# Performance work log

Measured on AMD Instinct MI355X. Metric: run time of the kernel, lower is better.

## Reference

```python
import jax, jax.numpy as jnp
import numpy as np

N, D = 8192, 128
ALPHA = 2.0


def setup_inputs() -> dict:
    key = jax.random.key(0)
    k1, k2, k3, k4 = jax.random.split(key, 4)
    z_au = jax.random.normal(k1, (N, D), dtype=jnp.float32)
    z_tp = jax.random.normal(k2, (N, D), dtype=jnp.float32)
    fc_weights = jax.random.normal(k3, (2, D), dtype=jnp.float32)
    labels = jax.random.randint(k4, (N,), 0, 2, dtype=jnp.int64)
    return {"z_au": z_au, "z_tp": z_tp, "fc_weights": fc_weights, "labels": labels}


def reference(z_au, z_tp, fc_weights, labels):
    # labels is unused in the (intended) math; kept for signature fidelity.
    n = z_au.shape[0]
    neg_inf = jnp.finfo(z_au.dtype).min
    eye = jnp.eye(n, dtype=bool)

    # pairwise dot-product similarities (cosim == raw matmul in the source)
    s_aa = z_au @ z_au.T              # [n, n]
    s_tt = z_tp @ z_tp.T              # [n, n]
    s_at = z_au @ z_tp.T              # [n, n]

    # pos_loss(i) = log( sum_{j!=i} exp(au_i.au_j) + exp(tp_i.tp_j) )
    pos_logits = jnp.concatenate(
        [jnp.where(eye, neg_inf, s_aa), jnp.where(eye, neg_inf, s_tt)], axis=1
    )                                  # [n, 2n]
    pos = jax.nn.logsumexp(pos_logits, axis=1)          # [n]

    # neg_loss(i) = log( sum_{j!=i} exp(au_i.tp_j) )
    neg = jax.nn.logsumexp(jnp.where(eye, neg_inf, s_at), axis=1)  # [n]

    # alpha * cosim(au_i, tp_i)
    au_tp_diag = jnp.einsum("nd,nd->n", z_au, z_tp)      # [n]

    supcon = jnp.sum(-pos + neg + ALPHA * au_tp_diag)

    # prototype loss: reward same-class prototype, punish other-class prototype
    pt0, pt1 = fc_weights[0], fc_weights[1]
    pt_loss = jnp.sum(-z_au @ pt0 + z_au @ pt1 - z_tp @ pt1 + z_tp @ pt0) / n

    return (pt_loss + supcon) / (n + 2)
```

## Files before the change

### kernel.cpp

```cpp
#include <hip/hip_runtime.h>


typedef float f32x4 __attribute__((ext_vector_type(4)));
typedef __bf16 bf16x8 __attribute__((ext_vector_type(8)));

static constexpr int   N_ROWS = 8192;
static constexpr int   DIM    = 128;
static constexpr float SQRT_LOG2E = 1.2011224087864498f;
static constexpr float C2  = 32.0f;
static constexpr float LN2 = 0.6931471805599453f;


__device__ inline unsigned short f2bf_rne(float x) {
    unsigned u = __builtin_bit_cast(unsigned, x);
    u += 0x7fffu + ((u >> 16) & 1u);
    return (unsigned short)(u >> 16);
}

__global__ void prep_kernel(const float* __restrict__ zau,
                            const float* __restrict__ ztp,
                            unsigned short* __restrict__ bau,
                            unsigned short* __restrict__ btp,
                            float* __restrict__ P, float* __restrict__ Ng,
                            float* __restrict__ acc) {
    int gid  = blockIdx.x * blockDim.x + threadIdx.x;
    int base = gid * 4;
    float4 a = *reinterpret_cast<const float4*>(zau + base);
    float4 t = *reinterpret_cast<const float4*>(ztp + base);
    ushort4 ua, ut;
    ua.x = f2bf_rne(a.x * SQRT_LOG2E); ua.y = f2bf_rne(a.y * SQRT_LOG2E);
    ua.z = f2bf_rne(a.z * SQRT_LOG2E); ua.w = f2bf_rne(a.w * SQRT_LOG2E);
    ut.x = f2bf_rne(t.x * SQRT_LOG2E); ut.y = f2bf_rne(t.y * SQRT_LOG2E);
    ut.z = f2bf_rne(t.z * SQRT_LOG2E); ut.w = f2bf_rne(t.w * SQRT_LOG2E);
    *reinterpret_cast<ushort4*>(bau + base) = ua;
    *reinterpret_cast<ushort4*>(btp + base) = ut;
    if (gid < N_ROWS) { P[gid] = 0.0f; Ng[gid] = 0.0f; }
    if (gid == 0)     { acc[0] = 0.0f; acc[1] = 0.0f; }
}

template<bool DIAG>
__device__ inline void accum_exp(const f32x4 (&acc)[2][4], float (&dst)[2][4],
                                 int r0w, int colbase, int quad, int l15) {
#pragma unroll
    for (int mt = 0; mt < 2; mt++)
#pragma unroll
        for (int nt = 0; nt < 4; nt++)
#pragma unroll
            for (int r = 0; r < 4; r++) {
                float e = __builtin_amdgcn_exp2f(acc[mt][nt][r]);
                if (DIAG) {
                    int grow = r0w + mt * 16 + quad * 4 + r;
                    int gcol = colbase + nt * 16 + l15;
                    if (grow == gcol) e = 0.0f;
                }
                dst[mt][r] += e;
            }
}

__global__ __launch_bounds__(256, 2)
void score_kernel(const unsigned short* __restrict__ bau,
                  const unsigned short* __restrict__ btp,
                  float* __restrict__ P, float* __restrict__ Ng) {
    __shared__ __align__(16) unsigned short ldsA[64 * 136];
    __shared__ __align__(16) unsigned short ldsT[64 * 136];

    const int tid  = threadIdx.x;
    const int lane = tid & 63;
    const int wave = tid >> 6;
    const int quad = lane >> 4;
    const int l15  = lane & 15;
    const int rb   = blockIdx.x >> 3;
    const int cs   = blockIdx.x & 7;
    const int r0w  = rb * 128 + wave * 32;

    bf16x8 aAu[2][4], aTp[2][4];
#pragma unroll
    for (int mt = 0; mt < 2; mt++) {
        int row = r0w + mt * 16 + l15;
        const unsigned short* pa = bau + row * DIM + quad * 8;
        const unsigned short* pt = btp + row * DIM + quad * 8;
#pragma unroll
        for (int k = 0; k < 4; k++) {
            aAu[mt][k] = *reinterpret_cast<const bf16x8*>(pa + k * 32);
            aTp[mt][k] = *reinterpret_cast<const bf16x8*>(pt + k * 32);
        }
    }

    float sP[2][4] = {{0.f,0.f,0.f,0.f},{0.f,0.f,0.f,0.f}};
    float sN[2][4] = {{0.f,0.f,0.f,0.f},{0.f,0.f,0.f,0.f}};

    for (int ct = 0; ct < 16; ct++) {
        const int colbase = cs * 1024 + ct * 64;
        __syncthreads();
#pragma unroll
        for (int j = 0; j < 8; j++) {
            int c   = tid + j * 256;
            int arr = c >> 10;
            int rem = c & 1023;
            int row = rem >> 4;
            int c16 = rem & 15;
            const unsigned short* src =
                (arr ? btp : bau) + (colbase + row) * DIM + c16 * 8;
            unsigned short* dst = (arr ? ldsT : ldsA) + row * 136 + c16 * 8;
            *reinterpret_cast<bf16x8*>(dst) =
                *reinterpret_cast<const bf16x8*>(src);
        }
        __syncthreads();

        const bool diag = (colbase < r0w + 32) && (colbase + 64 > r0w);

        {
            f32x4 acc[2][4];
#pragma unroll
            for (int mt = 0; mt < 2; mt++)
#pragma unroll
                for (int nt = 0; nt < 4; nt++)
                    acc[mt][nt] = f32x4{-C2, -C2, -C2, -C2};
#pragma unroll
            for (int k = 0; k < 4; k++) {
                bf16x8 b[4];
#pragma unroll
                for (int nt = 0; nt < 4; nt++)
                    b[nt] = *reinterpret_cast<const bf16x8*>(
                        ldsA + (nt * 16 + l15) * 136 + k * 32 + quad * 8);
#pragma unroll
                for (int nt = 0; nt < 4; nt++)
#pragma unroll
                    for (int mt = 0; mt < 2; mt++)
                        acc[mt][nt] = __builtin_amdgcn_mfma_f32_16x16x32_bf16(
                            aAu[mt][k], b[nt], acc[mt][nt], 0, 0, 0);
            }
            if (diag) accum_exp<true >(acc, sP, r0w, colbase, quad, l15);
            else      accum_exp<false>(acc, sP, r0w, colbase, quad, l15);
        }

        {
            f32x4 accT[2][4], accX[2][4];
#pragma unroll
            for (int mt = 0; mt < 2; mt++)
#pragma unroll
                for (int nt = 0; nt < 4; nt++) {
                    accT[mt][nt] = f32x4{-C2, -C2, -C2, -C2};
                    accX[mt][nt] = f32x4{-C2, -C2, -C2, -C2};
                }
#pragma unroll
            for (int k = 0; k < 4; k++) {
                bf16x8 b[4];
#pragma unroll
                for (int nt = 0; nt < 4; nt++)
                    b[nt] = *reinterpret_cast<const bf16x8*>(
                        ldsT + (nt * 16 + l15) * 136 + k * 32 + quad * 8);
#pragma unroll
                for (int nt = 0; nt < 4; nt++)
#pragma unroll
                    for (int mt = 0; mt < 2; mt++) {
                        accT[mt][nt] = __builtin_amdgcn_mfma_f32_16x16x32_bf16(
                            aTp[mt][k], b[nt], accT[mt][nt], 0, 0, 0);
                        accX[mt][nt] = __builtin_amdgcn_mfma_f32_16x16x32_bf16(
                            aAu[mt][k], b[nt], accX[mt][nt], 0, 0, 0);
                    }
            }
            if (diag) { accum_exp<true >(accT, sP, r0w, colbase, quad, l15);
                        accum_exp<true >(accX, sN, r0w, colbase, quad, l15); }
            else      { accum_exp<false>(accT, sP, r0w, colbase, quad, l15);
                        accum_exp<false>(accX, sN, r0w, colbase, quad, l15); }
        }
    }

#pragma unroll
    for (int mt = 0; mt < 2; mt++)
#pragma unroll
        for (int r = 0; r < 4; r++) {
            float p = sP[mt][r], ng = sN[mt][r];
            for (int m = 1; m < 16; m <<= 1) {
                p  += __shfl_xor(p,  m, 64);
                ng += __shfl_xor(ng, m, 64);
            }
            if (l15 == 0) {
                int row = r0w + mt * 16 + quad * 4 + r;
                atomicAdd(&P[row],  p);
                atomicAdd(&Ng[row], ng);
            }
        }
}

__global__ void finalize_kernel(const float* __restrict__ zau,
                                const float* __restrict__ ztp,
                                const float* __restrict__ fc,
                                const float* __restrict__ P,
                                const float* __restrict__ Ng,
                                float* __restrict__ acc) {
    int tid     = threadIdx.x;
    int lane    = tid & 63;
    int wave_id = blockIdx.x * 4 + (tid >> 6);

    float2 w0 = *reinterpret_cast<const float2*>(fc + 2 * lane);
    float2 w1 = *reinterpret_cast<const float2*>(fc + 256 + 2 * lane);
    float wx = w1.x - w0.x, wy = w1.y - w0.y;

    float ptp = 0.0f, ssum = 0.0f;
    for (int j = 0; j < 8; j++) {
        int i = wave_id * 8 + j;
        float2 a = *reinterpret_cast<const float2*>(zau + i * DIM + 2 * lane);
        float2 t = *reinterpret_cast<const float2*>(ztp + i * DIM + 2 * lane);
        float d = a.x * t.x + a.y * t.y;
        ptp += (a.x - t.x) * wx + (a.y - t.y) * wy;
        for (int m = 1; m < 64; m <<= 1) d += __shfl_xor(d, m, 64);
        if (lane == 0) {
            float c = LN2 * (__builtin_amdgcn_logf(Ng[i]) -
                             __builtin_amdgcn_logf(P[i])) + 2.0f * d;
            ssum += c;
        }
    }
    for (int m = 1; m < 64; m <<= 1) ptp += __shfl_xor(ptp, m, 64);
    if (lane == 0) {
        atomicAdd(&acc[0], ssum);
        atomicAdd(&acc[1], ptp);
    }
}

__global__ void write_out_kernel(const float* __restrict__ acc,
                                 float* __restrict__ out) {
    out[0] = (acc[1] / (float)N_ROWS + acc[0]) / (float)(N_ROWS + 2);
}

extern "C" void kernel_launch(void* const* d_in, const int* in_sizes, int n_in,
                              void* d_out, int out_size, void* d_ws, size_t ws_size,
                              hipStream_t stream) {
    const float* zau = (const float*)d_in[0];
    const float* ztp = (const float*)d_in[1];
    const float* fc  = (const float*)d_in[2];
    float* out = (float*)d_out;

    char* ws = (char*)d_ws;
    unsigned short* bau = (unsigned short*)(ws);
    unsigned short* btp = (unsigned short*)(ws + 2097152);
    float* P   = (float*)(ws + 4194304);
    float* Ng  = (float*)(ws + 4227072);
    float* acc = (float*)(ws + 4259840);

    prep_kernel<<<dim3(1024), dim3(256), 0, stream>>>(zau, ztp, bau, btp, P, Ng, acc);
    score_kernel<<<dim3(512), dim3(256), 0, stream>>>(bau, btp, P, Ng);
    finalize_kernel<<<dim3(256), dim3(256), 0, stream>>>(zau, ztp, fc, P, Ng, acc);
    write_out_kernel<<<dim3(1), dim3(1), 0, stream>>>(acc, out);
}
```

Measured before the change: 155.0 us.

## Load score tiles via global_load_lds in MFMA layout, split grid finer, fuse final write

Column tiles are now copied straight from global memory into LDS with global_load_lds, laid out in the MFMA fragment order so each lane reads its B operand contiguously instead of through a padded row stride. The grid doubles to 1024 blocks, each covering 512 columns, with occupancy raised to 3 blocks per CU and the block-to-row mapping changed so row blocks vary fastest. MFMA work per column tile is split into two 32-column halves to lower register pressure. The final write_out launch is folded into finalize through a last-block ticket counter, which saves one launch but adds an atomic and a fence.

Result: slower. 158.4 us (+2.2%).

```diff
diff --git a/kernel.cpp b/kernel.cpp
--- a/kernel.cpp
+++ b/kernel.cpp
@@ -17,12 +17,17 @@
     return (unsigned short)(u >> 16);
 }
 
+#define GLD16(gptr, lptr)                                                  \
+    __builtin_amdgcn_global_load_lds(                                      \
+        (const __attribute__((address_space(1))) void*)(gptr),             \
+        (__attribute__((address_space(3))) void*)(lptr), 16, 0, 0)
+
 __global__ void prep_kernel(const float* __restrict__ zau,
                             const float* __restrict__ ztp,
                             unsigned short* __restrict__ bau,
                             unsigned short* __restrict__ btp,
                             float* __restrict__ P, float* __restrict__ Ng,
-                            float* __restrict__ acc) {
+                            float* __restrict__ acc, unsigned* __restrict__ done) {
     int gid  = blockIdx.x * blockDim.x + threadIdx.x;
     int base = gid * 4;
     float4 a = *reinterpret_cast<const float4*>(zau + base);
@@ -35,43 +40,46 @@
     *reinterpret_cast<ushort4*>(bau + base) = ua;
     *reinterpret_cast<ushort4*>(btp + base) = ut;
     if (gid < N_ROWS) { P[gid] = 0.0f; Ng[gid] = 0.0f; }
-    if (gid == 0)     { acc[0] = 0.0f; acc[1] = 0.0f; }
+    if (gid == 0)     { acc[0] = 0.0f; acc[1] = 0.0f; done[0] = 0u; }
 }
 
 template<bool DIAG>
-__device__ inline void accum_exp(const f32x4 (&acc)[2][4], float (&dst)[2][4],
-                                 int r0w, int colbase, int quad, int l15) {
+__device__ inline void accum2(const f32x4 (&a)[2][2], float (&dst)[2][4],
+                              int r0w, int colp, int quad, int l15) {
 #pragma unroll
     for (int mt = 0; mt < 2; mt++)
 #pragma unroll
-        for (int nt = 0; nt < 4; nt++)
+        for (int nt = 0; nt < 2; nt++)
 #pragma unroll
             for (int r = 0; r < 4; r++) {
-                float e = __builtin_amdgcn_exp2f(acc[mt][nt][r]);
+                float e = __builtin_amdgcn_exp2f(a[mt][nt][r]);
                 if (DIAG) {
                     int grow = r0w + mt * 16 + quad * 4 + r;
-                    int gcol = colbase + nt * 16 + l15;
+                    int gcol = colp + nt * 16 + l15;
                     if (grow == gcol) e = 0.0f;
                 }
                 dst[mt][r] += e;
             }
 }
 
-__global__ __launch_bounds__(256, 2)
+__global__ __launch_bounds__(256, 3)
 void score_kernel(const unsigned short* __restrict__ bau,
                   const unsigned short* __restrict__ btp,
                   float* __restrict__ P, float* __restrict__ Ng) {
-    __shared__ __align__(16) unsigned short ldsA[64 * 136];
-    __shared__ __align__(16) unsigned short ldsT[64 * 136];
+    __shared__ __align__(16) unsigned short ldsA[16 * 512];
+    __shared__ __align__(16) unsigned short ldsT[16 * 512];
 
     const int tid  = threadIdx.x;
     const int lane = tid & 63;
     const int wave = tid >> 6;
     const int quad = lane >> 4;
     const int l15  = lane & 15;
-    const int rb   = blockIdx.x >> 3;
-    const int cs   = blockIdx.x & 7;
+    const int rb   = blockIdx.x & 63;
+    const int cs   = blockIdx.x >> 6;
     const int r0w  = rb * 128 + wave * 32;
+
+    const int laneoff = l15 * 256 + quad * 16;
+
 
     bf16x8 aAu[2][4], aTp[2][4];
 #pragma unroll
@@ -89,81 +97,82 @@
     float sP[2][4] = {{0.f,0.f,0.f,0.f},{0.f,0.f,0.f,0.f}};
     float sN[2][4] = {{0.f,0.f,0.f,0.f},{0.f,0.f,0.f,0.f}};
 
-    for (int ct = 0; ct < 16; ct++) {
-        const int colbase = cs * 1024 + ct * 64;
+    for (int ct = 0; ct < 8; ct++) {
+        const int colbase = cs * 512 + ct * 64;
         __syncthreads();
 #pragma unroll
         for (int j = 0; j < 8; j++) {
-            int c   = tid + j * 256;
-            int arr = c >> 10;
-            int rem = c & 1023;
-            int row = rem >> 4;
-            int c16 = rem & 15;
-            const unsigned short* src =
-                (arr ? btp : bau) + (colbase + row) * DIM + c16 * 8;
-            unsigned short* dst = (arr ? ldsT : ldsA) + row * 136 + c16 * 8;
-            *reinterpret_cast<bf16x8*>(dst) =
-                *reinterpret_cast<const bf16x8*>(src);
+            const int f   = wave * 8 + j;
+            const int arr = f >> 4;
+            const int nt  = (f >> 2) & 3;
+            const int k   = f & 3;
+            const char* gb = (const char*)(arr ? btp : bau)
+                           + ((size_t)(colbase + nt * 16) << 8) + (k << 6);
+            unsigned short* lb = (arr ? ldsT : ldsA) + ((nt * 4 + k) << 9);
+            GLD16(gb + laneoff, lb);
         }
         __syncthreads();
 
         const bool diag = (colbase < r0w + 32) && (colbase + 64 > r0w);
 
-        {
-            f32x4 acc[2][4];
+#pragma unroll
+        for (int np = 0; np < 2; np++) {
+            f32x4 acc[2][2];
 #pragma unroll
             for (int mt = 0; mt < 2; mt++)
 #pragma unroll
-                for (int nt = 0; nt < 4; nt++)
+                for (int nt = 0; nt < 2; nt++)
                     acc[mt][nt] = f32x4{-C2, -C2, -C2, -C2};
 #pragma unroll
             for (int k = 0; k < 4; k++) {
-                bf16x8 b[4];
-#pragma unroll
-                for (int nt = 0; nt < 4; nt++)
-                    b[nt] = *reinterpret_cast<const bf16x8*>(
-                        ldsA + (nt * 16 + l15) * 136 + k * 32 + quad * 8);
-#pragma unroll
-                for (int nt = 0; nt < 4; nt++)
-#pragma unroll
-                    for (int mt = 0; mt < 2; mt++)
-                        acc[mt][nt] = __builtin_amdgcn_mfma_f32_16x16x32_bf16(
-                            aAu[mt][k], b[nt], acc[mt][nt], 0, 0, 0);
-            }
-            if (diag) accum_exp<true >(acc, sP, r0w, colbase, quad, l15);
-            else      accum_exp<false>(acc, sP, r0w, colbase, quad, l15);
-        }
-
-        {
-            f32x4 accT[2][4], accX[2][4];
+                bf16x8 b0 = *reinterpret_cast<const bf16x8*>(
+                    ldsA + (((np * 2 + 0) * 4 + k) << 9) + lane * 8);
+                bf16x8 b1 = *reinterpret_cast<const bf16x8*>(
+                    ldsA + (((np * 2 + 1) * 4 + k) << 9) + lane * 8);
+#pragma unroll
+                for (int mt = 0; mt < 2; mt++) {
+                    acc[mt][0] = __builtin_amdgcn_mfma_f32_16x16x32_bf16(
+                        aAu[mt][k], b0, acc[mt][0], 0, 0, 0);
+                    acc[mt][1] = __builtin_amdgcn_mfma_f32_16x16x32_bf16(
+                        aAu[mt][k], b1, acc[mt][1], 0, 0, 0);
+                }
+            }
+            if (diag) accum2<true >(acc, sP, r0w, colbase + np * 32, quad, l15);
+            else      accum2<false>(acc, sP, r0w, colbase + np * 32, quad, l15);
+        }
+
+#pragma unroll
+        for (int np = 0; np < 2; np++) {
+            f32x4 aT[2][2], aX[2][2];
 #pragma unroll
             for (int mt = 0; mt < 2; mt++)
 #pragma unroll
-                for (int nt = 0; nt < 4; nt++) {
-                    accT[mt][nt] = f32x4{-C2, -C2, -C2, -C2};
-                    accX[mt][nt] = f32x4{-C2, -C2, -C2, -C2};
+                for (int nt = 0; nt < 2; nt++) {
+                    aT[mt][nt] = f32x4{-C2, -C2, -C2, -C2};
+                    aX[mt][nt] = f32x4{-C2, -C2, -C2, -C2};
                 }
 #pragma unroll
             for (int k = 0; k < 4; k++) {
-                bf16x8 b[4];
-#pragma unroll
-                for (int nt = 0; nt < 4; nt++)
-                    b[nt] = *reinterpret_cast<const bf16x8*>(
-                        ldsT + (nt * 16 + l15) * 136 + k * 32 + quad * 8);
-#pragma unroll
-                for (int nt = 0; nt < 4; nt++)
-#pragma unroll
-                    for (int mt = 0; mt < 2; mt++) {
-                        accT[mt][nt] = __builtin_amdgcn_mfma_f32_16x16x32_bf16(
-                            aTp[mt][k], b[nt], accT[mt][nt], 0, 0, 0);
-                        accX[mt][nt] = __builtin_amdgcn_mfma_f32_16x16x32_bf16(
-                            aAu[mt][k], b[nt], accX[mt][nt], 0, 0, 0);
-                    }
-            }
-            if (diag) { accum_exp<true >(accT, sP, r0w, colbase, quad, l15);
-                        accum_exp<true >(accX, sN, r0w, colbase, quad, l15); }
-            else      { accum_exp<false>(accT, sP, r0w, colbase, quad, l15);
-                        accum_exp<false>(accX, sN, r0w, colbase, quad, l15); }
+                bf16x8 b0 = *reinterpret_cast<const bf16x8*>(
+                    ldsT + (((np * 2 + 0) * 4 + k) << 9) + lane * 8);
+                bf16x8 b1 = *reinterpret_cast<const bf16x8*>(
+                    ldsT + (((np * 2 + 1) * 4 + k) << 9) + lane * 8);
+#pragma unroll
+                for (int mt = 0; mt < 2; mt++) {
+                    aT[mt][0] = __builtin_amdgcn_mfma_f32_16x16x32_bf16(
+                        aTp[mt][k], b0, aT[mt][0], 0, 0, 0);
+                    aX[mt][0] = __builtin_amdgcn_mfma_f32_16x16x32_bf16(
+                        aAu[mt][k], b0, aX[mt][0], 0, 0, 0);
+                    aT[mt][1] = __builtin_amdgcn_mfma_f32_16x16x32_bf16(
+                        aTp[mt][k], b1, aT[mt][1], 0, 0, 0);
+                    aX[mt][1] = __builtin_amdgcn_mfma_f32_16x16x32_bf16(
+                        aAu[mt][k], b1, aX[mt][1], 0, 0, 0);
+                }
+            }
+            if (diag) { accum2<true >(aT, sP, r0w, colbase + np * 32, quad, l15);
+                        accum2<true >(aX, sN, r0w, colbase + np * 32, quad, l15); }
+            else      { accum2<false>(aT, sP, r0w, colbase + np * 32, quad, l15);
+                        accum2<false>(aX, sN, r0w, colbase + np * 32, quad, l15); }
         }
     }
 
@@ -189,7 +198,9 @@
                                 const float* __restrict__ fc,
                                 const float* __restrict__ P,
                                 const float* __restrict__ Ng,
-                                float* __restrict__ acc) {
+                                float* __restrict__ acc,
+                                unsigned* __restrict__ done,
+                                float* __restrict__ out) {
     int tid     = threadIdx.x;
     int lane    = tid & 63;
     int wave_id = blockIdx.x * 4 + (tid >> 6);
@@ -217,11 +228,17 @@
         atomicAdd(&acc[0], ssum);
         atomicAdd(&acc[1], ptp);
     }
-}
-
-__global__ void write_out_kernel(const float* __restrict__ acc,
-                                 float* __restrict__ out) {
-    out[0] = (acc[1] / (float)N_ROWS + acc[0]) / (float)(N_ROWS + 2);
+
+    __syncthreads();
+    if (tid == 0) {
+        __threadfence();
+        unsigned ticket = atomicAdd(done, 1u);
+        if (ticket == gridDim.x - 1) {
+            float a0 = atomicAdd(&acc[0], 0.0f);
+            float a1 = atomicAdd(&acc[1], 0.0f);
+            out[0] = (a1 / (float)N_ROWS + a0) / (float)(N_ROWS + 2);
+        }
+    }
 }
 
 extern "C" void kernel_launch(void* const* d_in, const int* in_sizes, int n_in,
@@ -235,12 +252,12 @@
     char* ws = (char*)d_ws;
     unsigned short* bau = (unsigned short*)(ws);
     unsigned short* btp = (unsigned short*)(ws + 2097152);
-    float* P   = (float*)(ws + 4194304);
-    float* Ng  = (float*)(ws + 4227072);
-    float* acc = (float*)(ws + 4259840);
-
-    prep_kernel<<<dim3(1024), dim3(256), 0, stream>>>(zau, ztp, bau, btp, P, Ng, acc);
-    score_kernel<<<dim3(512), dim3(256), 0, stream>>>(bau, btp, P, Ng);
-    finalize_kernel<<<dim3(256), dim3(256), 0, stream>>>(zau, ztp, fc, P, Ng, acc);
-    write_out_kernel<<<dim3(1), dim3(1), 0, stream>>>(acc, out);
-}
+    float*    P    = (float*)(ws + 4194304);
+    float*    Ng   = (float*)(ws + 4227072);
+    float*    acc  = (float*)(ws + 4259840);
+    unsigned* done = (unsigned*)(ws + 4259848);
+
+    prep_kernel<<<dim3(1024), dim3(256), 0, stream>>>(zau, ztp, bau, btp, P, Ng, acc, done);
+    score_kernel<<<dim3(1024), dim3(256), 0, stream>>>(bau, btp, P, Ng);
+    finalize_kernel<<<dim3(256), dim3(256), 0, stream>>>(zau, ztp, fc, P, Ng, acc, done, out);
+}
```
